# Kernel optimization log

Measured on AMD Instinct MI355X. Metric: run time of the kernel, lower is better.

The kernel has to match this reference:

```python
import jax, jax.numpy as jnp
import numpy as np

# model constants (match init_kwargs)
NC, N, D, A, P = 64, 256, 64, 4, 4      # cells, neurons/cell, D_n, alpha, border_per_cell
GH, GW, G = 8, 8, 8                      # grid, mlp groups
HS, HM, HMOD, MOD_OUT = 256, 256, 64, 5  # state/msg/mod hidden dims, mod outputs
BS = 16
K_INIT = 16
# port layout: input [0:A), output [A:2A), border [2A:2A+P)


def setup_inputs() -> dict:
    key = jax.random.key(0)
    ks = jax.random.split(key, 16)
    f = lambda k, s: jax.random.normal(k, s, dtype=jnp.float32)
    inp = {}
    inp['x'] = f(ks[0], (BS, NC * D))
    inp['h'] = f(ks[1], (BS, NC, N, D)) * 0.01
    inp['msg'] = f(ks[2], (BS, NC, N, D)) * 0.01
    # sparse-valued dense connectivity: ~K_INIT nonzeros (0.1) per row, zero diagonal
    mask = (jax.random.uniform(ks[3], (BS, NC, N, N)) < K_INIT / N).astype(jnp.float32)
    inp['W'] = 0.1 * mask * (1.0 - jnp.eye(N, dtype=jnp.float32))
    inp['decay_logit'] = jnp.zeros((BS, NC, N), jnp.float32)
    inp['cell_context'] = f(ks[4], (BS, NC, D)) * 0.01
    inp['border_gate_logit'] = jnp.zeros((BS, NC, P), jnp.float32)
    # learned parameters
    inp['neuron_id'] = f(ks[5], (NC, N, D)) * 0.02
    inp['state_w1'] = f(ks[6], (HS, 2 * D)) * 0.05
    inp['state_b1'] = jnp.zeros((HS,), jnp.float32)
    inp['state_w2'] = f(ks[7], (D, HS)) * 0.01
    inp['state_b2'] = jnp.zeros((D,), jnp.float32)
    inp['msg_w1'] = f(ks[8], (HM, D)) * 0.05
    inp['msg_b1'] = jnp.zeros((HM,), jnp.float32)
    inp['msg_w2'] = f(ks[9], (D, HM)) * 0.01
    inp['msg_b2'] = jnp.zeros((D,), jnp.float32)
    inp['inject_w'] = f(ks[10], (G, A * D, D)) * 0.05
    inp['inject_b'] = jnp.zeros((G, A * D), jnp.float32)
    inp['mod_w1'] = f(ks[11], (NC, D, HMOD)) * 0.05
    inp['mod_b1'] = jnp.zeros((NC, HMOD), jnp.float32)
    inp['mod_w2'] = f(ks[12], (NC, HMOD, MOD_OUT)) * 0.001
    inp['mod_b2'] = jnp.zeros((NC, MOD_OUT), jnp.float32)
    inp['cell_to_group'] = jnp.arange(NC, dtype=jnp.int32) % G
    return inp


def reference(x, h, msg, W, decay_logit, cell_context, border_gate_logit,
              neuron_id, state_w1, state_b1, state_w2, state_b2,
              msg_w1, msg_b1, msg_w2, msg_b2, inject_w, inject_b,
              mod_w1, mod_b1, mod_w2, mod_b2, cell_to_group):
    B = x.shape[0]
    # per-cell modulation MLP (mod_w1/mod_w2 indexed by cell) -> decay / border gates
    hid = jnp.tanh(jnp.einsum('bcd,cdh->bch', cell_context, mod_w1) + mod_b1)
    mod = jnp.einsum('bch,cho->bco', hid, mod_w2) + mod_b2        # (B,NC,MOD_OUT)
    decay = jax.nn.sigmoid(decay_logit + mod[:, :, 0:1])          # (B,NC,N)
    bgate = jax.nn.sigmoid(border_gate_logit + mod[:, :, 1:1 + P])  # (B,NC,P)
    # _receive: dense matmul message passing, received = W @ msg
    received = jnp.einsum('bcnm,bcmd->bcnd', W, msg)
    # _inject: group-indexed projection of external input into input ports
    iw = inject_w[cell_to_group]                                  # (NC, A*D, D)
    ib = inject_b[cell_to_group]                                  # (NC, A*D)
    cell_x = x.reshape(B, NC, D)
    inj = (jnp.einsum('bci,coi->bco', cell_x, iw) + ib).reshape(B, NC, A, D)
    received = received.at[:, :, 0:A].add(inj)
    # _border_exchange: fixed geometric grid shifts of border ports
    border = msg[:, :, 2 * A:2 * A + P].reshape(B, GH, GW, P, D)
    incoming = jnp.zeros_like(border)
    incoming = incoming.at[:, 1:, :, 0].set(border[:, :-1, :, 1])
    incoming = incoming.at[:, :-1, :, 1].set(border[:, 1:, :, 0])
    incoming = incoming.at[:, :, 1:, 2].set(border[:, :, :-1, 3])
    incoming = incoming.at[:, :, :-1, 3].set(border[:, :, 1:, 2])
    incoming = incoming.reshape(B, NC, P, D)
    received = received.at[:, :, 2 * A:2 * A + P].add(bgate[..., None] * incoming)
    # _state_update: split first layer (avoids cat([received, h]))
    w1_recv, w1_h = state_w1[:, :D], state_w1[:, D:]
    hid_s = jnp.tanh(received @ w1_recv.T + h @ w1_h.T + state_b1)
    cand = jnp.tanh(hid_s @ state_w2.T + state_b2)                # (B,NC,N,D)
    d = decay[..., None]
    h_new = d * h + (1.0 - d) * cand
    # _emit_message: two-layer tanh MLP + neuron identity
    hid_m = jnp.tanh(h_new @ msg_w1.T + msg_b1)
    msg_new = jnp.tanh(hid_m @ msg_w2.T + msg_b2) + neuron_id[None]
    # _readout: mean over output ports, flattened per cell
    readout = msg_new[:, :, A:2 * A].mean(axis=2).reshape(B, NC * D)
    return readout, h_new, msg_new
```

## Files before the change

### kernel.cpp

```cpp
#include <hip/hip_runtime.h>
#include <math.h>

#define BB 16
#define NCC 64
#define NN 256
#define DD 64

typedef short s16x8 __attribute__((ext_vector_type(8)));
typedef float f32x4 __attribute__((ext_vector_type(4)));

#define MFMA16(a,b,c) __builtin_amdgcn_mfma_f32_16x16x32_bf16((a),(b),(c),0,0,0)

__device__ __forceinline__ unsigned short f2bf(float f){
    union{float f;unsigned u;}v; v.f=f;
    unsigned r = v.u + 0x7FFFu + ((v.u>>16)&1u);
    return (unsigned short)(r>>16);
}
__device__ __forceinline__ float bf2f(unsigned short s){
    union{unsigned u;float f;}v; v.u=((unsigned)s)<<16; return v.f;
}
__device__ __forceinline__ unsigned cvt2(float a,float b){
    unsigned r;
    asm("v_cvt_pk_bf16_f32 %0, %1, %2" : "=v"(r) : "v"(a), "v"(b));
    return r;
}
__device__ __forceinline__ unsigned short cvt1(float a){
    unsigned r;
    asm("v_cvt_pk_bf16_f32 %0, %1, %2" : "=v"(r) : "v"(a), "v"(a));
    return (unsigned short)r;
}
__device__ __forceinline__ s16x8 pack8(float4 lo,float4 hi){
    union{unsigned u[4];s16x8 v;}r;
    r.u[0]=cvt2(lo.x,lo.y); r.u[1]=cvt2(lo.z,lo.w);
    r.u[2]=cvt2(hi.x,hi.y); r.u[3]=cvt2(hi.z,hi.w);
    return r.v;
}
__device__ __forceinline__ float tanh2(float x){
    float e = __builtin_amdgcn_exp2f(x * 2.8853900817779268f);
    return 1.0f - 2.0f * __builtin_amdgcn_rcpf(e + 1.0f);
}
__device__ __forceinline__ float sigm(float v){ return __builtin_amdgcn_rcpf(1.0f+__expf(-v)); }

extern "C" __global__ void __launch_bounds__(256)
wconv(const float* __restrict__ sw1, const float* __restrict__ sw2,
      const float* __restrict__ mw1, const float* __restrict__ mw2,
      unsigned short* __restrict__ ws)
{
    const int i = blockIdx.x * 256 + threadIdx.x;
    float v;
    if (i < 32768)      v = sw1[i];
    else if (i < 49152) v = sw2[i - 32768];
    else if (i < 65536) v = mw1[i - 49152];
    else                v = mw2[i - 65536];
    ws[i] = f2bf(v);
}

extern "C" __global__ void __launch_bounds__(512,2)
mg_recv(const float* __restrict__ x, const float* __restrict__ msg,
        const float* __restrict__ W, const float* __restrict__ decay_logit,
        const float* __restrict__ cell_context, const float* __restrict__ border_gate_logit,
        const float* __restrict__ inject_w, const float* __restrict__ inject_b,
        const float* __restrict__ mod_w1, const float* __restrict__ mod_b1,
        const float* __restrict__ mod_w2, const float* __restrict__ mod_b2,
        const int* __restrict__ cell_to_group,
        unsigned short* __restrict__ ws_recv, float* __restrict__ ws_decay)
{
    __shared__ __align__(16) float s_w[2][32*260];
    __shared__ __align__(16) unsigned short s_msgT[64*264];
    __shared__ float s_x[64], s_cc[64], s_hmod[64], s_mod[8], s_bgate[4];
    __shared__ float s_inj[256], s_bord[256];

    const int tid  = threadIdx.x;
    const int lane = tid & 63;
    const int l15  = lane & 15;
    const int g    = lane >> 4;
    const int wid  = __builtin_amdgcn_readfirstlane(tid >> 6);
    const int bc   = blockIdx.x;
    const int b    = bc >> 6;
    const int c    = bc & 63;
    const float* Wb = W + (size_t)bc * NN * NN;

#define STAGE_CHUNK(n) do{                                                            \
    const int _buf=(n)&1;                                                             \
    _Pragma("unroll")                                                                 \
    for(int _j=0;_j<4;++_j){                                                          \
        const int _row=4*wid+_j;                                                      \
        const float* _gp = Wb + (size_t)(32*(n)+_row)*NN + lane*4;                    \
        __builtin_amdgcn_global_load_lds(                                             \
            (const __attribute__((address_space(1))) void*)_gp,                       \
            (__attribute__((address_space(3))) void*)&s_w[_buf][_row*260], 16, 0, 0); \
    }                                                                                 \
}while(0)

    STAGE_CHUNK(0);
    STAGE_CHUNK(1);

    for (int it = tid; it < 2048; it += 512) {
        const int d4 = it & 15, mp = it >> 4;
        const float* src = msg + ((size_t)bc * NN + mp * 2) * DD + d4 * 4;
        const float4 v0 = *(const float4*)(src);
        const float4 v1 = *(const float4*)(src + DD);
        const float* p0 = &v0.x; const float* p1 = &v1.x;
        #pragma unroll
        for (int j = 0; j < 4; ++j)
            *(unsigned*)&s_msgT[(d4 * 4 + j) * 264 + mp * 2] = cvt2(p0[j], p1[j]);
    }

    asm volatile("s_waitcnt lgkmcnt(0)" ::: "memory");
    __builtin_amdgcn_sched_barrier(0);
    __builtin_amdgcn_s_barrier();
    __builtin_amdgcn_sched_barrier(0);

    const int rt = wid & 1, ct = wid >> 1;
    for (int rc = 0; rc < 8; ++rc) {
        if (rc >= 1 && rc <= 6) STAGE_CHUNK(rc + 1);
        if (rc < 7) asm volatile("s_waitcnt vmcnt(4)" ::: "memory");
        else        asm volatile("s_waitcnt vmcnt(0)" ::: "memory");
        __builtin_amdgcn_sched_barrier(0);
        __builtin_amdgcn_s_barrier();
        __builtin_amdgcn_sched_barrier(0);
        {
            const float* wrow = &s_w[rc & 1][(16 * rt + l15) * 260];
            const unsigned short* brow = &s_msgT[(16 * ct + l15) * 264];
            f32x4 acc = {0.f, 0.f, 0.f, 0.f};
            #pragma unroll
            for (int k = 0; k < 8; ++k) {
                const float4 w0 = *(const float4*)(wrow + 32 * k + 8 * g);
                const float4 w1 = *(const float4*)(wrow + 32 * k + 8 * g + 4);
                const s16x8 bf = *(const s16x8*)(brow + 32 * k + 8 * g);
                acc = MFMA16(pack8(w0, w1), bf, acc);
            }
            const int rowb = 32 * rc + 16 * rt + 4 * g;
            unsigned short* op = ws_recv + ((size_t)bc * NN + rowb) * DD + 16 * ct + l15;
            #pragma unroll
            for (int i = 0; i < 4; ++i) op[i * DD] = cvt1(acc[i]);
        }
        __builtin_amdgcn_sched_barrier(0);
        __builtin_amdgcn_s_barrier();
        __builtin_amdgcn_sched_barrier(0);
    }
#undef STAGE_CHUNK

    if (tid < 64) {
        s_cc[tid] = cell_context[bc * DD + tid];
        s_x[tid]  = x[(size_t)b * (NCC * DD) + c * DD + tid];
    }
    __syncthreads();
    if (tid < 64) {
        float acc = mod_b1[c * 64 + tid];
        const float* wp = mod_w1 + (size_t)c * 64 * 64 + tid;
        #pragma unroll
        for (int d = 0; d < 64; ++d) acc += s_cc[d] * wp[d * 64];
        s_hmod[tid] = tanh2(acc);
    }
    __syncthreads();
    if (tid < 5) {
        float acc = mod_b2[c * 5 + tid];
        const float* wp = mod_w2 + (size_t)c * 64 * 5 + tid;
        #pragma unroll
        for (int hh = 0; hh < 64; ++hh) acc += s_hmod[hh] * wp[hh * 5];
        s_mod[tid] = acc;
    }
    __syncthreads();
    if (tid < 256) {
        ws_decay[bc * NN + tid] = sigm(decay_logit[(size_t)bc * NN + tid] + s_mod[0]);
        if (tid < 4) s_bgate[tid] = sigm(border_gate_logit[bc * 4 + tid] + s_mod[1 + tid]);
    }
    __syncthreads();
    if (tid < 256) {
        const int grp = cell_to_group[c];
        float acc = inject_b[grp * 256 + tid];
        const float4* wv = (const float4*)(inject_w + ((size_t)grp * 256 + tid) * 64);
        #pragma unroll
        for (int i4 = 0; i4 < 16; ++i4) {
            const float4 v = wv[i4];
            acc += v.x * s_x[i4 * 4 + 0] + v.y * s_x[i4 * 4 + 1]
                 + v.z * s_x[i4 * 4 + 2] + v.w * s_x[i4 * 4 + 3];
        }
        s_inj[tid] = acc;
    } else {
        const int q = tid - 256, p = q >> 6, d = q & 63;
        const int gi = c >> 3, gj = c & 7;
        int cn = -1, ps = 0;
        if (p == 0)      { if (gi > 0) { cn = c - 8; ps = 1; } }
        else if (p == 1) { if (gi < 7) { cn = c + 8; ps = 0; } }
        else if (p == 2) { if (gj > 0) { cn = c - 1; ps = 3; } }
        else             { if (gj < 7) { cn = c + 1; ps = 2; } }
        s_bord[q] = (cn >= 0) ? s_bgate[p] * msg[(((size_t)b * NCC + cn) * NN + 8 + ps) * DD + d]
                              : 0.0f;
    }
    __syncthreads();
    if (tid < 256) {
        const int n = tid >> 6, d = tid & 63;
        unsigned short* base = ws_recv + (size_t)bc * NN * DD;
        unsigned short* p1 = base + n * DD + d;
        *p1 = f2bf(bf2f(*p1) + s_inj[tid]);
        unsigned short* p2 = base + (8 + n) * DD + d;
        *p2 = f2bf(bf2f(*p2) + s_bord[tid]);
    }
}

extern "C" __global__ void __launch_bounds__(256,2)
mg_mlp(const float* __restrict__ h, const float* __restrict__ neuron_id,
       const float* __restrict__ state_b1, const float* __restrict__ state_b2,
       const float* __restrict__ msg_b1, const float* __restrict__ msg_b2,
       const unsigned short* __restrict__ sw1b, const unsigned short* __restrict__ sw2b,
       const unsigned short* __restrict__ mw1b, const unsigned short* __restrict__ mw2b,
       const unsigned short* __restrict__ ws_recv, const float* __restrict__ ws_decay,
       float* __restrict__ out_read, float* __restrict__ out_h, float* __restrict__ out_msg)
{
    __shared__ __align__(16) unsigned short s_hid[64*264];
    __shared__ __align__(16) unsigned short s_h[64*72];
    __shared__ float s_mn[256];

    const int tid = threadIdx.x, lane = tid & 63, l15 = lane & 15, g = lane >> 4;
    const int wid = __builtin_amdgcn_readfirstlane(tid >> 6);
    const int bx = blockIdx.x, tile = bx & 3, bc = bx >> 2, b = bc >> 6, c = bc & 63;
    const int row0 = tile * 64;

    s16x8 ar0[4], ar1[4], ah0[4], ah1[4];
    #pragma unroll
    for (int rt = 0; rt < 4; ++rt) {
        const unsigned short* rrow = ws_recv + ((size_t)bc * NN + row0 + 16 * rt + l15) * DD;
        ar0[rt] = *(const s16x8*)(rrow + 8 * g);
        ar1[rt] = *(const s16x8*)(rrow + 32 + 8 * g);
        const float* hrow = h + ((size_t)bc * NN + row0 + 16 * rt + l15) * DD;
        ah0[rt] = pack8(*(const float4*)(hrow + 8 * g),      *(const float4*)(hrow + 8 * g + 4));
        ah1[rt] = pack8(*(const float4*)(hrow + 32 + 8 * g), *(const float4*)(hrow + 36 + 8 * g));
    }
    s16x8 wB[16];
    float biasB[4];
    #pragma unroll
    for (int cc = 0; cc < 4; ++cc) {
        const unsigned short* Bb = sw1b + (size_t)(64 * wid + 16 * cc + l15) * 128;
        wB[cc * 4 + 0] = *(const s16x8*)(Bb + 8 * g);
        wB[cc * 4 + 1] = *(const s16x8*)(Bb + 32 + 8 * g);
        wB[cc * 4 + 2] = *(const s16x8*)(Bb + 64 + 8 * g);
        wB[cc * 4 + 3] = *(const s16x8*)(Bb + 96 + 8 * g);
        biasB[cc] = state_b1[64 * wid + 16 * cc + l15];
    }

    #pragma unroll
    for (int cc = 0; cc < 4; ++cc) {
        const int n0 = 64 * wid + 16 * cc;
        #pragma unroll
        for (int rt = 0; rt < 4; ++rt) {
            f32x4 acc = {0.f, 0.f, 0.f, 0.f};
            acc = MFMA16(ar0[rt], wB[cc * 4 + 0], acc);
            acc = MFMA16(ar1[rt], wB[cc * 4 + 1], acc);
            acc = MFMA16(ah0[rt], wB[cc * 4 + 2], acc);
            acc = MFMA16(ah1[rt], wB[cc * 4 + 3], acc);
            #pragma unroll
            for (int i = 0; i < 4; ++i)
                s_hid[(16 * rt + 4 * g + i) * 264 + n0 + l15] = cvt1(tanh2(acc[i] + biasB[cc]));
        }
    }
    __syncthreads();

    {
        const int d0 = 16 * wid + l15;
        const unsigned short* B0 = sw2b + (size_t)d0 * 256;
        s16x8 wf[8];
        #pragma unroll
        for (int k = 0; k < 8; ++k) wf[k] = *(const s16x8*)(B0 + 32 * k + 8 * g);
        const float sb = state_b2[d0];
        float hvv[16], dcc[16];
        #pragma unroll
        for (int rt = 0; rt < 4; ++rt)
            #pragma unroll
            for (int i = 0; i < 4; ++i) {
                const int grow = row0 + 16 * rt + 4 * g + i;
                hvv[rt * 4 + i] = h[((size_t)bc * NN + grow) * DD + d0];
                dcc[rt * 4 + i] = ws_decay[bc * NN + grow];
            }
        #pragma unroll
        for (int rt = 0; rt < 4; ++rt) {
            f32x4 acc = {0.f, 0.f, 0.f, 0.f};
            #pragma unroll
            for (int k = 0; k < 8; ++k) {
                const s16x8 af = *(const s16x8*)&s_hid[(16 * rt + l15) * 264 + 32 * k + 8 * g];
                acc = MFMA16(af, wf[k], acc);
            }
            #pragma unroll
            for (int i = 0; i < 4; ++i) {
                const int lrow = 16 * rt + 4 * g + i, grow = row0 + lrow;
                const float dec = dcc[rt * 4 + i];
                const float hn  = dec * hvv[rt * 4 + i] + (1.0f - dec) * tanh2(acc[i] + sb);
                s_h[lrow * 72 + d0] = cvt1(hn);
                out_h[((size_t)bc * NN + grow) * DD + d0] = hn;
            }
        }
    }
    __syncthreads();

    {
        s16x8 hn0[4], hn1[4];
        #pragma unroll
        for (int rt = 0; rt < 4; ++rt) {
            const int hr = (16 * rt + l15) * 72;
            hn0[rt] = *(const s16x8*)&s_h[hr + 8 * g];
            hn1[rt] = *(const s16x8*)&s_h[hr + 32 + 8 * g];
        }
        s16x8 wD[8];
        float biasD[4];
        #pragma unroll
        for (int cc = 0; cc < 4; ++cc) {
            const unsigned short* Bb = mw1b + (size_t)(64 * wid + 16 * cc + l15) * 64;
            wD[cc * 2 + 0] = *(const s16x8*)(Bb + 8 * g);
            wD[cc * 2 + 1] = *(const s16x8*)(Bb + 32 + 8 * g);
            biasD[cc] = msg_b1[64 * wid + 16 * cc + l15];
        }
        #pragma unroll
        for (int cc = 0; cc < 4; ++cc) {
            const int n0 = 64 * wid + 16 * cc;
            #pragma unroll
            for (int rt = 0; rt < 4; ++rt) {
                f32x4 acc = {0.f, 0.f, 0.f, 0.f};
                acc = MFMA16(hn0[rt], wD[cc * 2 + 0], acc);
                acc = MFMA16(hn1[rt], wD[cc * 2 + 1], acc);
                #pragma unroll
                for (int i = 0; i < 4; ++i)
                    s_hid[(16 * rt + 4 * g + i) * 264 + n0 + l15] = cvt1(tanh2(acc[i] + biasD[cc]));
            }
        }
    }
    __syncthreads();

    {
        const int d0 = 16 * wid + l15;
        const unsigned short* B0 = mw2b + (size_t)d0 * 256;
        s16x8 wf[8];
        #pragma unroll
        for (int k = 0; k < 8; ++k) wf[k] = *(const s16x8*)(B0 + 32 * k + 8 * g);
        const float mb = msg_b2[d0];
        float nid[16];
        #pragma unroll
        for (int rt = 0; rt < 4; ++rt)
            #pragma unroll
            for (int i = 0; i < 4; ++i)
                nid[rt * 4 + i] = neuron_id[((size_t)c * NN + row0 + 16 * rt + 4 * g + i) * DD + d0];
        #pragma unroll
        for (int rt = 0; rt < 4; ++rt) {
            f32x4 acc = {0.f, 0.f, 0.f, 0.f};
            #pragma unroll
            for (int k = 0; k < 8; ++k) {
                const s16x8 af = *(const s16x8*)&s_hid[(16 * rt + l15) * 264 + 32 * k + 8 * g];
                acc = MFMA16(af, wf[k], acc);
            }
            #pragma unroll
            for (int i = 0; i < 4; ++i) {
                const int lrow = 16 * rt + 4 * g + i, grow = row0 + lrow;
                const float m = tanh2(acc[i] + mb) + nid[rt * 4 + i];
                out_msg[((size_t)bc * NN + grow) * DD + d0] = m;
                if (tile == 0 && lrow >= 4 && lrow < 8) s_mn[(lrow - 4) * 64 + d0] = m;
            }
        }
    }
    __syncthreads();
    if (tile == 0 && tid < 64)
        out_read[(size_t)b * (NCC * DD) + c * 64 + tid] =
            0.25f * (s_mn[tid] + s_mn[64 + tid] + s_mn[128 + tid] + s_mn[192 + tid]);
}

extern "C" void kernel_launch(void* const* d_in, const int* in_sizes, int n_in,
                              void* d_out, int out_size, void* d_ws, size_t ws_size,
                              hipStream_t stream) {
    (void)in_sizes; (void)n_in; (void)ws_size; (void)out_size;
    const float* x                 = (const float*)d_in[0];
    const float* h                 = (const float*)d_in[1];
    const float* msg               = (const float*)d_in[2];
    const float* W                 = (const float*)d_in[3];
    const float* decay_logit       = (const float*)d_in[4];
    const float* cell_context      = (const float*)d_in[5];
    const float* border_gate_logit = (const float*)d_in[6];
    const float* neuron_id         = (const float*)d_in[7];
    const float* state_w1          = (const float*)d_in[8];
    const float* state_b1          = (const float*)d_in[9];
    const float* state_w2          = (const float*)d_in[10];
    const float* state_b2          = (const float*)d_in[11];
    const float* msg_w1            = (const float*)d_in[12];
    const float* msg_b1            = (const float*)d_in[13];
    const float* msg_w2            = (const float*)d_in[14];
    const float* msg_b2            = (const float*)d_in[15];
    const float* inject_w          = (const float*)d_in[16];
    const float* inject_b          = (const float*)d_in[17];
    const float* mod_w1            = (const float*)d_in[18];
    const float* mod_b1            = (const float*)d_in[19];
    const float* mod_w2            = (const float*)d_in[20];
    const float* mod_b2            = (const float*)d_in[21];
    const int*   cell_to_group     = (const int*)d_in[22];

    float* out_read = (float*)d_out;
    float* out_h    = out_read + (size_t)BB * NCC * DD;
    float* out_msg  = out_h + (size_t)BB * NCC * NN * DD;

    unsigned short* ws16   = (unsigned short*)d_ws;
    unsigned short* sw1b   = ws16;
    unsigned short* sw2b   = ws16 + 32768;
    unsigned short* mw1b   = ws16 + 49152;
    unsigned short* mw2b   = ws16 + 65536;
    float*          ws_dec = (float*)((char*)d_ws + 163840);
    unsigned short* ws_rcv = (unsigned short*)((char*)d_ws + 1212416);

    hipLaunchKernelGGL(wconv, dim3(320), dim3(256), 0, stream,
                       state_w1, state_w2, msg_w1, msg_w2, ws16);

    hipLaunchKernelGGL(mg_recv, dim3(BB * NCC), dim3(512), 0, stream,
                       x, msg, W, decay_logit, cell_context, border_gate_logit,
                       inject_w, inject_b, mod_w1, mod_b1, mod_w2, mod_b2,
                       cell_to_group, ws_rcv, ws_dec);

    hipLaunchKernelGGL(mg_mlp, dim3(BB * NCC * 4), dim3(256), 0, stream,
                       h, neuron_id, state_b1, state_b2, msg_b1, msg_b2,
                       sw1b, sw2b, mw1b, mw2b, ws_rcv, ws_dec,
                       out_read, out_h, out_msg);
}
```

Baseline: 243.0 us.

## Split mg_mlp work across eight waves per block to cut register pressure

The MLP kernel now runs 512 threads per block instead of 256. The hidden-dimension columns (layers 1 and 3) are split across 8 waves, and the output columns and row tiles (layers 2 and 4) are split across wave pairs. Each wave holds half as many weight fragments and accumulators, so VGPR use drops and occupancy should rise under the new launch bounds of 512,6. In exchange, each wave still loads all A fragments (recv/h) redundantly in layer 1, and the same amount of work is coordinated by more waves.

```diff
diff --git a/kernel.cpp b/kernel.cpp
--- a/kernel.cpp
+++ b/kernel.cpp
@@ -200,7 +200,7 @@
     }
 }
 
-extern "C" __global__ void __launch_bounds__(256,2)
+extern "C" __global__ void __launch_bounds__(512,6)
 mg_mlp(const float* __restrict__ h, const float* __restrict__ neuron_id,
        const float* __restrict__ state_b1, const float* __restrict__ state_b2,
        const float* __restrict__ msg_b1, const float* __restrict__ msg_b2,
@@ -215,6 +215,7 @@
 
     const int tid = threadIdx.x, lane = tid & 63, l15 = lane & 15, g = lane >> 4;
     const int wid = __builtin_amdgcn_readfirstlane(tid >> 6);
+    const int wc = wid >> 1, wr = wid & 1;
     const int bx = blockIdx.x, tile = bx & 3, bc = bx >> 2, b = bc >> 6, c = bc & 63;
     const int row0 = tile * 64;
 
@@ -228,21 +229,21 @@
         ah0[rt] = pack8(*(const float4*)(hrow + 8 * g),      *(const float4*)(hrow + 8 * g + 4));
         ah1[rt] = pack8(*(const float4*)(hrow + 32 + 8 * g), *(const float4*)(hrow + 36 + 8 * g));
     }
-    s16x8 wB[16];
-    float biasB[4];
+    s16x8 wB[8];
+    float biasB[2];
     #pragma unroll
-    for (int cc = 0; cc < 4; ++cc) {
-        const unsigned short* Bb = sw1b + (size_t)(64 * wid + 16 * cc + l15) * 128;
+    for (int cc = 0; cc < 2; ++cc) {
+        const unsigned short* Bb = sw1b + (size_t)(32 * wid + 16 * cc + l15) * 128;
         wB[cc * 4 + 0] = *(const s16x8*)(Bb + 8 * g);
         wB[cc * 4 + 1] = *(const s16x8*)(Bb + 32 + 8 * g);
         wB[cc * 4 + 2] = *(const s16x8*)(Bb + 64 + 8 * g);
         wB[cc * 4 + 3] = *(const s16x8*)(Bb + 96 + 8 * g);
-        biasB[cc] = state_b1[64 * wid + 16 * cc + l15];
+        biasB[cc] = state_b1[32 * wid + 16 * cc + l15];
     }
 
     #pragma unroll
-    for (int cc = 0; cc < 4; ++cc) {
-        const int n0 = 64 * wid + 16 * cc;
+    for (int cc = 0; cc < 2; ++cc) {
+        const int n0 = 32 * wid + 16 * cc;
         #pragma unroll
         for (int rt = 0; rt < 4; ++rt) {
             f32x4 acc = {0.f, 0.f, 0.f, 0.f};
@@ -258,23 +259,26 @@
     __syncthreads();
 
     {
-        const int d0 = 16 * wid + l15;
+        const int d0 = 16 * wc + l15;
         const unsigned short* B0 = sw2b + (size_t)d0 * 256;
         s16x8 wf[8];
         #pragma unroll
         for (int k = 0; k < 8; ++k) wf[k] = *(const s16x8*)(B0 + 32 * k + 8 * g);
         const float sb = state_b2[d0];
-        float hvv[16], dcc[16];
-        #pragma unroll
-        for (int rt = 0; rt < 4; ++rt)
+        float hvv[8], dcc[8];
+        #pragma unroll
+        for (int rtl = 0; rtl < 2; ++rtl) {
+            const int rt = 2 * wr + rtl;
             #pragma unroll
             for (int i = 0; i < 4; ++i) {
                 const int grow = row0 + 16 * rt + 4 * g + i;
-                hvv[rt * 4 + i] = h[((size_t)bc * NN + grow) * DD + d0];
-                dcc[rt * 4 + i] = ws_decay[bc * NN + grow];
-            }
-        #pragma unroll
-        for (int rt = 0; rt < 4; ++rt) {
+                hvv[rtl * 4 + i] = h[((size_t)bc * NN + grow) * DD + d0];
+                dcc[rtl * 4 + i] = ws_decay[bc * NN + grow];
+            }
+        }
+        #pragma unroll
+        for (int rtl = 0; rtl < 2; ++rtl) {
+            const int rt = 2 * wr + rtl;
             f32x4 acc = {0.f, 0.f, 0.f, 0.f};
             #pragma unroll
             for (int k = 0; k < 8; ++k) {
@@ -284,8 +288,8 @@
             #pragma unroll
             for (int i = 0; i < 4; ++i) {
                 const int lrow = 16 * rt + 4 * g + i, grow = row0 + lrow;
-                const float dec = dcc[rt * 4 + i];
-                const float hn  = dec * hvv[rt * 4 + i] + (1.0f - dec) * tanh2(acc[i] + sb);
+                const float dec = dcc[rtl * 4 + i];
+                const float hn  = dec * hvv[rtl * 4 + i] + (1.0f - dec) * tanh2(acc[i] + sb);
                 s_h[lrow * 72 + d0] = cvt1(hn);
                 out_h[((size_t)bc * NN + grow) * DD + d0] = hn;
             }
@@ -301,18 +305,18 @@
             hn0[rt] = *(const s16x8*)&s_h[hr + 8 * g];
             hn1[rt] = *(const s16x8*)&s_h[hr + 32 + 8 * g];
         }
-        s16x8 wD[8];
-        float biasD[4];
-        #pragma unroll
-        for (int cc = 0; cc < 4; ++cc) {
-            const unsigned short* Bb = mw1b + (size_t)(64 * wid + 16 * cc + l15) * 64;
+        s16x8 wD[4];
+        float biasD[2];
+        #pragma unroll
+        for (int cc = 0; cc < 2; ++cc) {
+            const unsigned short* Bb = mw1b + (size_t)(32 * wid + 16 * cc + l15) * 64;
             wD[cc * 2 + 0] = *(const s16x8*)(Bb + 8 * g);
             wD[cc * 2 + 1] = *(const s16x8*)(Bb + 32 + 8 * g);
-            biasD[cc] = msg_b1[64 * wid + 16 * cc + l15];
-        }
-        #pragma unroll
-        for (int cc = 0; cc < 4; ++cc) {
-            const int n0 = 64 * wid + 16 * cc;
+            biasD[cc] = msg_b1[32 * wid + 16 * cc + l15];
+        }
+        #pragma unroll
+        for (int cc = 0; cc < 2; ++cc) {
+            const int n0 = 32 * wid + 16 * cc;
             #pragma unroll
             for (int rt = 0; rt < 4; ++rt) {
                 f32x4 acc = {0.f, 0.f, 0.f, 0.f};
@@ -327,20 +331,23 @@
     __syncthreads();
 
     {
-        const int d0 = 16 * wid + l15;
+        const int d0 = 16 * wc + l15;
         const unsigned short* B0 = mw2b + (size_t)d0 * 256;
         s16x8 wf[8];
         #pragma unroll
         for (int k = 0; k < 8; ++k) wf[k] = *(const s16x8*)(B0 + 32 * k + 8 * g);
         const float mb = msg_b2[d0];
-        float nid[16];
-        #pragma unroll
-        for (int rt = 0; rt < 4; ++rt)
+        float nid[8];
+        #pragma unroll
+        for (int rtl = 0; rtl < 2; ++rtl) {
+            const int rt = 2 * wr + rtl;
             #pragma unroll
             for (int i = 0; i < 4; ++i)
-                nid[rt * 4 + i] = neuron_id[((size_t)c * NN + row0 + 16 * rt + 4 * g + i) * DD + d0];
-        #pragma unroll
-        for (int rt = 0; rt < 4; ++rt) {
+                nid[rtl * 4 + i] = neuron_id[((size_t)c * NN + row0 + 16 * rt + 4 * g + i) * DD + d0];
+        }
+        #pragma unroll
+        for (int rtl = 0; rtl < 2; ++rtl) {
+            const int rt = 2 * wr + rtl;
             f32x4 acc = {0.f, 0.f, 0.f, 0.f};
             #pragma unroll
             for (int k = 0; k < 8; ++k) {
@@ -350,7 +357,7 @@
             #pragma unroll
             for (int i = 0; i < 4; ++i) {
                 const int lrow = 16 * rt + 4 * g + i, grow = row0 + lrow;
-                const float m = tanh2(acc[i] + mb) + nid[rt * 4 + i];
+                const float m = tanh2(acc[i] + mb) + nid[rtl * 4 + i];
                 out_msg[((size_t)bc * NN + grow) * DD + d0] = m;
                 if (tile == 0 && lrow >= 4 && lrow < 8) s_mn[(lrow - 4) * 64 + d0] = m;
             }
@@ -410,7 +417,7 @@
                        inject_w, inject_b, mod_w1, mod_b1, mod_w2, mod_b2,
                        cell_to_group, ws_rcv, ws_dec);
 
-    hipLaunchKernelGGL(mg_mlp, dim3(BB * NCC * 4), dim3(256), 0, stream,
+    hipLaunchKernelGGL(mg_mlp, dim3(BB * NCC * 4), dim3(512), 0, stream,
                        h, neuron_id, state_b1, state_b2, msg_b1, msg_b2,
                        sw1b, sw2b, mw1b, mw2b, ws_rcv, ws_dec,
                        out_read, out_h, out_msg);
```

After: 376.3 us. 1.55x slower.
